# Optimization experiments

Measured on AMD Instinct MI355X. Metric: run time of the kernel, lower is better.

## Reference

```python
import jax, jax.numpy as jnp
import numpy as np

NUM_CODES = 1024
DIM = 64
COMMITMENT_WEIGHT = 0.25
SOFT_TEMP = 1.0


def setup_inputs() -> dict:
    key = jax.random.key(0)
    k1, k2 = jax.random.split(key)
    z = jax.random.normal(k1, (32, 4096, DIM), dtype=jnp.float32)
    codebook = jax.random.normal(k2, (NUM_CODES, DIM), dtype=jnp.float32)
    return {"z": z, "codebook": codebook}


def reference(z, codebook):
    b, k, d = z.shape
    flat = z.reshape(-1, d)  # [N, d]
    # squared euclidean distances [N, num_codes]
    distances = (
        jnp.sum(flat * flat, axis=1, keepdims=True)
        - 2.0 * flat @ codebook.T
        + jnp.sum(codebook * codebook, axis=1)[None, :]
    )
    indices = jnp.argmin(distances, axis=1)  # [N]
    logits = -distances / max(SOFT_TEMP, 1e-06)
    probs = jax.nn.softmax(logits, axis=1)

    quantized = codebook[indices].reshape(b, k, d)
    # use_ema=True -> quantized is detached from graph
    quantized = jax.lax.stop_gradient(quantized)

    codebook_loss = jnp.mean((jax.lax.stop_gradient(quantized) - z) ** 2)
    commitment_loss = jnp.mean((quantized - jax.lax.stop_gradient(z)) ** 2)
    loss = codebook_loss + COMMITMENT_WEIGHT * commitment_loss

    # straight-through estimator
    quantized_st = z + jax.lax.stop_gradient(quantized - z)

    counts = jnp.zeros((NUM_CODES,), dtype=jnp.float32).at[indices].add(1.0)
    usage = counts / jnp.maximum(counts.sum(), 1.0)
    soft_usage = probs.mean(axis=0)
    perplexity = jnp.exp(-jnp.sum(usage * jnp.log(usage + 1e-08)))

    return (
        quantized_st,
        loss,
        indices.reshape(b, k),
        codebook_loss,
        commitment_loss,
        perplexity,
        usage,
        soft_usage,
    )
```

## Files before the change

kernel.cpp:

```cpp
#include <hip/hip_runtime.h>

constexpr int K = 1024;
constexpr int D = 64;
constexpr int N = 131072;
constexpr float INV_N = 1.0f / 131072.0f;
constexpr float INV_ELEMS = 1.0f / 8388608.0f;
constexpr float LOG2E = 1.4426950408889634f;
constexpr float DELTA = 0.0072f;

constexpr size_t O_QST  = 0;
constexpr size_t O_LOSS = 8388608;
constexpr size_t O_IDX  = 8388609;
constexpr size_t O_CBL  = 8519681;
constexpr size_t O_CML  = 8519682;
constexpr size_t O_PPL  = 8519683;
constexpr size_t O_USG  = 8519684;
constexpr size_t O_SU   = 8520708;



typedef __attribute__((ext_vector_type(8))) short bf16x8;
typedef __attribute__((ext_vector_type(16))) float f32x16;
typedef __attribute__((ext_vector_type(4))) float f32x4;

__device__ inline unsigned short f2bf(float f) {
  unsigned u = __float_as_uint(f);
  return (unsigned short)((u + 0x7FFF + ((u >> 16) & 1)) >> 16);
}
__device__ inline float bf2f(unsigned short h) {
  return __uint_as_float(((unsigned)h) << 16);
}
__device__ inline float fexp2(float x) {
  return __builtin_amdgcn_exp2f(x);
}
__device__ inline float fmed3(float a, float b, float c) {
  return __builtin_amdgcn_fmed3f(a, b, c);
}
__device__ inline bf16x8 negbf8(bf16x8 v) {
  union { bf16x8 s; uint4 u; } x;
  x.s = v;
  x.u.x ^= 0x80008000u; x.u.y ^= 0x80008000u;
  x.u.z ^= 0x80008000u; x.u.w ^= 0x80008000u;
  return x.s;
}

__global__ __launch_bounds__(256) void vq_prep(const float* __restrict__ cb,
                                               short* __restrict__ chA,
                                               short* __restrict__ clA,
                                               float* __restrict__ cn,
                                               float* __restrict__ cn2f) {
  const int gid = blockIdx.x * 256 + threadIdx.x;
  const int c = gid >> 6, d = gid & 63;
  float raw = cb[gid];
  float v = raw * LOG2E;
  unsigned short h = f2bf(v);
  unsigned short l = f2bf(v - bf2f(h));
  const int tile = c >> 5, ks = d >> 4, hff = (d >> 3) & 1, j = d & 7;
  const int lane = hff * 32 + (c & 31);
  const size_t off = ((size_t)((tile * 4 + ks) * 64 + lane)) * 8 + j;
  chA[off] = (short)h;
  clA[off] = (short)l;
  float s = raw * raw;
#pragma unroll
  for (int o = 32; o > 0; o >>= 1) s += __shfl_xor(s, o, 64);
  if (d == 0) {
    cn[c] = s;
    cn2f[c] = s * LOG2E;
  }
}

__global__ __launch_bounds__(256, 4) void vq_p1(
    const float* __restrict__ z, const short* __restrict__ chA,
    const short* __restrict__ clA, const float* __restrict__ cn2f,
    float* __restrict__ out, float* __restrict__ ctA,
    int* __restrict__ wl) {
  const int lane = threadIdx.x & 63;
  const int W = blockIdx.x * 4 + (threadIdx.x >> 6);
  const int i0 = W * 32;
  const int col = lane & 31;
  const int hf = lane >> 5;

  bf16x8 zh[4], zl[4];
  const float* zr = z + (size_t)(i0 + col) * 64 + hf * 8;
#pragma unroll
  for (int ks = 0; ks < 4; ks++) {
    float4 a = *(const float4*)(zr + ks * 16);
    float4 b = *(const float4*)(zr + ks * 16 + 4);
    float vv[8] = {a.x, a.y, a.z, a.w, b.x, b.y, b.z, b.w};
#pragma unroll
    for (int j = 0; j < 8; j++) {
      float vm = -2.0f * vv[j];
      unsigned short h = f2bf(vm);
      zh[ks][j] = (short)h;
      zl[ks][j] = (short)f2bf(vm - bf2f(h));
    }
  }
  {
    short* base = (short*)out + (size_t)W * 4096;
#pragma unroll
    for (int ks = 0; ks < 4; ks++) {
      *(bf16x8*)(base + (ks * 64 + lane) * 8) = zh[ks];
      *(bf16x8*)(base + 2048 + (ks * 64 + lane) * 8) = zl[ks];
    }
  }

  float b1 = 3.0e38f, b2 = 3.0e38f, Z = 0.0f;
  int bi = 0;

  for (int t = 0; t < 32; t++) {
    float4 cniv[4];
#pragma unroll
    for (int q = 0; q < 4; q++)
      cniv[q] = *(const float4*)(cn2f + t * 32 + 8 * q + 4 * hf);
    f32x16 acc;
#pragma unroll
    for (int r = 0; r < 16; r++)
      acc[r] = ((const float*)&cniv[r >> 2])[r & 3];
    const short* ch = chA + ((size_t)(t * 4) * 64 + lane) * 8;
    const short* cl = clA + ((size_t)(t * 4) * 64 + lane) * 8;
#pragma unroll
    for (int ks = 0; ks < 4; ks++) {
      bf16x8 Ah = *(const bf16x8*)(ch + ks * 512);
      bf16x8 Al = *(const bf16x8*)(cl + ks * 512);
      acc = __builtin_amdgcn_mfma_f32_32x32x16_bf16(Ah, zh[ks], acc, 0, 0, 0);
      acc = __builtin_amdgcn_mfma_f32_32x32x16_bf16(Ah, zl[ks], acc, 0, 0, 0);
      acc = __builtin_amdgcn_mfma_f32_32x32x16_bf16(Al, zh[ks], acc, 0, 0, 0);
    }
    float pm[8], px[8];
#pragma unroll
    for (int r = 0; r < 8; r++) {
      pm[r] = fminf(acc[2 * r], acc[2 * r + 1]);
      px[r] = fmaxf(acc[2 * r], acc[2 * r + 1]);
    }
    float qm[4], qx[4];
#pragma unroll
    for (int r = 0; r < 4; r++) {
      qm[r] = fminf(pm[2 * r], pm[2 * r + 1]);
      qx[r] = fmed3(pm[2 * r], pm[2 * r + 1], fminf(px[2 * r], px[2 * r + 1]));
    }
    float rm0 = fminf(qm[0], qm[1]);
    float rx0 = fmed3(qm[0], qm[1], fminf(qx[0], qx[1]));
    float rm1 = fminf(qm[2], qm[3]);
    float rx1 = fmed3(qm[2], qm[3], fminf(qx[2], qx[3]));
    float cm = fminf(rm0, rm1);
    float cm2 = fmed3(rm0, rm1, fminf(rx0, rx1));
    int ti = 0;
#pragma unroll
    for (int r = 0; r < 16; r++)
      if (acc[r] == cm) ti = t * 32 + (r & 3) + 8 * (r >> 2) + 4 * hf;
    float newm = fminf(b1, cm);
    b2 = fmed3(b1, cm, fminf(b2, cm2));
    bi = (cm < b1) ? ti : bi;
    float zs = 0.0f;
#pragma unroll
    for (int r = 0; r < 16; r++) zs += fexp2(newm - acc[r]);
    Z = Z * fexp2(newm - b1) + zs;
    b1 = newm;
  }
  float m2 = __shfl_xor(b1, 32, 64);
  float Z2 = __shfl_xor(Z, 32, 64);
  float b1o = m2;
  float b2o = __shfl_xor(b2, 32, 64);
  int bio = __shfl_xor(bi, 32, 64);
  float M = fminf(b1, m2);
  float Zt = Z * fexp2(M - b1) + Z2 * fexp2(M - m2);
  bool take = (b1o < b1) || (b1o == b1 && bio < bi);
  float g2 = fminf(fmaxf(b1, b1o), fminf(b2, b2o));
  int big = take ? bio : bi;
  if (hf == 0) {
    ctA[i0 + col] = M - __log2f(Zt);
    out[O_IDX + (size_t)(i0 + col)] = (float)big;
    if (g2 - M < DELTA) {
      int slot = atomicAdd(wl, 1);
      if (slot < 131071) wl[1 + slot] = i0 + col;
    }
  }
}

__global__ __launch_bounds__(256) void vq_count(
    const float* __restrict__ idxF, float* __restrict__ counts) {
  __shared__ int h[K];
  const int tid = threadIdx.x;
#pragma unroll
  for (int k = 0; k < K / 256; k++) h[tid + k * 256] = 0;
  __syncthreads();
  const int base = blockIdx.x * 2048 + tid;
#pragma unroll
  for (int k = 0; k < 8; k++) {
    int c = (int)idxF[base + k * 256];
    atomicAdd(&h[c], 1);
  }
  __syncthreads();
#pragma unroll
  for (int k = 0; k < K / 256; k++) {
    int v = h[tid + k * 256];
    if (v) atomicAdd(&counts[tid + k * 256], (float)v);
  }
}

__global__ __launch_bounds__(256, 4) void vq_p2(
    const short* __restrict__ zF, const short* __restrict__ chA,
    const short* __restrict__ clA, const float* __restrict__ cn2f,
    const float* __restrict__ ctA, float* __restrict__ susum) {
  const int lane = threadIdx.x & 63;
  const int wv = threadIdx.x >> 6;
  const int b = blockIdx.x;
  const int xcd = b & 7;
  const int sl = b >> 3;
  const int pg = xcd * 32 + (sl >> 3);
  const int g = (sl & 7) * 4 + wv;
  const int col = lane & 31;
  const int hf = lane >> 5;

  bf16x8 Bh[4], Bl[4];
  const short* ch = chA + ((size_t)(g * 4) * 64 + lane) * 8;
  const short* cl = clA + ((size_t)(g * 4) * 64 + lane) * 8;
#pragma unroll
  for (int ks = 0; ks < 4; ks++) {
    Bh[ks] = negbf8(*(const bf16x8*)(ch + ks * 512));
    Bl[ks] = negbf8(*(const bf16x8*)(cl + ks * 512));
  }
  const float cnv = cn2f[g * 32 + col];

  float su = 0.0f;
  for (int pt = 0; pt < 16; pt++) {
    const int T = pg * 16 + pt;
    const short* base = zF + (size_t)T * 4096;
    float4 ctv[4];
#pragma unroll
    for (int q = 0; q < 4; q++)
      ctv[q] = *(const float4*)(ctA + T * 32 + 8 * q + 4 * hf);
    f32x16 acc;
#pragma unroll
    for (int r = 0; r < 16; r++)
      acc[r] = ((const float*)&ctv[r >> 2])[r & 3] - cnv;
#pragma unroll
    for (int ks = 0; ks < 4; ks++) {
      bf16x8 Ah = *(const bf16x8*)(base + (ks * 64 + lane) * 8);
      bf16x8 Al = *(const bf16x8*)(base + 2048 + (ks * 64 + lane) * 8);
      acc = __builtin_amdgcn_mfma_f32_32x32x16_bf16(Ah, Bh[ks], acc, 0, 0, 0);
      acc = __builtin_amdgcn_mfma_f32_32x32x16_bf16(Ah, Bl[ks], acc, 0, 0, 0);
      acc = __builtin_amdgcn_mfma_f32_32x32x16_bf16(Al, Bh[ks], acc, 0, 0, 0);
    }
#pragma unroll
    for (int r = 0; r < 16; r++) su += fexp2(acc[r]);
  }
  su += __shfl_xor(su, 32, 64);
  if (hf == 0) atomicAdd(&susum[g * 32 + col], su);
}

__global__ __launch_bounds__(256) void vq_rescan(
    const float* __restrict__ z, const float* __restrict__ cb,
    const float* __restrict__ cn, float* __restrict__ out,
    float* __restrict__ counts, const int* __restrict__ wl) {
  const int nr = min(wl[0], 131071);
  const int wv = blockIdx.x * 4 + (threadIdx.x >> 6);
  const int lane = threadIdx.x & 63;
  for (int e = wv; e < nr; e += gridDim.x * 4) {
    const int i = wl[1 + e];
    const float4* zi4 = (const float4*)(z + (size_t)i * 64);
    float4 zq[16];
#pragma unroll
    for (int k = 0; k < 16; k++) zq[k] = zi4[k];
    float best = 3.0e38f;
    int bidx = 0;
    for (int cc = 0; cc < 16; cc++) {
      int c = cc * 64 + lane;
      const float4* cr = (const float4*)(cb + (size_t)c * 64);
      float dot0 = 0.0f, dot1 = 0.0f;
#pragma unroll
      for (int k = 0; k < 16; k += 2) {
        float4 a = cr[k];
        float4 bq = cr[k + 1];
        dot0 += zq[k].x * a.x + zq[k].y * a.y + zq[k].z * a.z + zq[k].w * a.w;
        dot1 += zq[k + 1].x * bq.x + zq[k + 1].y * bq.y + zq[k + 1].z * bq.z +
                zq[k + 1].w * bq.w;
      }
      float s = cn[c] - 2.0f * (dot0 + dot1);
      if (s < best) { best = s; bidx = c; }
    }
#pragma unroll
    for (int o = 32; o > 0; o >>= 1) {
      float ob = __shfl_xor(best, o, 64);
      int oi = __shfl_xor(bidx, o, 64);
      if (ob < best || (ob == best && oi < bidx)) { best = ob; bidx = oi; }
    }
    if (lane == 0) {
      const int old = (int)out[O_IDX + (size_t)i];
      if (bidx != old) {
        out[O_IDX + (size_t)i] = (float)bidx;
        atomicAdd(&counts[old], -1.0f);
        atomicAdd(&counts[bidx], 1.0f);
      }
    }
  }
}

__global__ __launch_bounds__(256) void vq_epi(
    const float* __restrict__ z, const float* __restrict__ cb,
    const float* __restrict__ idxF, float* __restrict__ qst,
    float* __restrict__ sqp) {
  const int tid = threadIdx.x;
  const int base = blockIdx.x * 2048 + tid;
  const int q = base & 15;
  int bI[8];
#pragma unroll
  for (int k = 0; k < 8; k++) bI[k] = (int)idxF[(base + k * 256) >> 4];
  f32x4 zv[8];
#pragma unroll
  for (int k = 0; k < 8; k++)
    zv[k] = __builtin_nontemporal_load((const f32x4*)z + base + k * 256);
  f32x4 qv[8];
#pragma unroll
  for (int k = 0; k < 8; k++) qv[k] = ((const f32x4*)cb)[bI[k] * 16 + q];
  float sq = 0.0f;
#pragma unroll
  for (int k = 0; k < 8; k++) {
    f32x4 o = zv[k] + (qv[k] - zv[k]);
    __builtin_nontemporal_store(o, (f32x4*)qst + base + k * 256);
    f32x4 e = qv[k] - zv[k];
    sq += e.x * e.x + e.y * e.y + e.z * e.z + e.w * e.w;
  }
#pragma unroll
  for (int o2 = 32; o2 > 0; o2 >>= 1) sq += __shfl_xor(sq, o2, 64);
  if ((tid & 63) == 0)
    atomicAdd(&sqp[(blockIdx.x * 4 + (tid >> 6)) & 255], sq);
}

__global__ __launch_bounds__(1024) void vq_final(
    const float* __restrict__ counts, const float* __restrict__ susum,
    const float* __restrict__ sqp, float* __restrict__ out) {
  __shared__ float red[16];
  __shared__ float red2[16];
  const int t = threadIdx.x;
  float cnt = counts[t];
  float usage = cnt * INV_N;
  out[O_USG + t] = usage;
  out[O_SU + t] = susum[t] * INV_N;
  float term = usage * logf(usage + 1e-8f);
  float sq = (t < 256) ? sqp[t] : 0.0f;
#pragma unroll
  for (int o = 32; o > 0; o >>= 1) {
    term += __shfl_xor(term, o, 64);
    sq += __shfl_xor(sq, o, 64);
  }
  if ((t & 63) == 0) {
    red[t >> 6] = term;
    red2[t >> 6] = sq;
  }
  __syncthreads();
  if (t < 16) {
    float v = red[t];
    float s2 = red2[t];
#pragma unroll
    for (int o = 8; o > 0; o >>= 1) {
      v += __shfl_xor(v, o, 64);
      s2 += __shfl_xor(s2, o, 64);
    }
    if (t == 0) {
      float ppl = __expf(-v);
      float cbl = s2 * INV_ELEMS;
      out[O_LOSS] = cbl + 0.25f * cbl;
      out[O_CBL] = cbl;
      out[O_CML] = cbl;
      out[O_PPL] = ppl;
    }
  }
}

extern "C" void kernel_launch(void* const* d_in, const int* in_sizes, int n_in,
                              void* d_out, int out_size, void* d_ws,
                              size_t ws_size, hipStream_t stream) {
  const float* z = (const float*)d_in[0];
  const float* cb = (const float*)d_in[1];
  float* ws = (float*)d_ws;
  float* cn = ws;
  float* counts = ws + 1024;
  float* susum = ws + 2048;
  float* sqp = ws + 3072;
  float* cn2f = ws + 3328;
  short* chA = (short*)(ws + 4352);
  short* clA = (short*)(ws + 37120);
  float* ctA = ws + 69888;
  int* wl = (int*)(ws + 200960);
  float* out = (float*)d_out;

  hipMemsetAsync(counts, 0, (1024 + 1024 + 256) * sizeof(float), stream);
  hipMemsetAsync(wl, 0, sizeof(int), stream);

  vq_prep<<<256, 256, 0, stream>>>(cb, chA, clA, cn, cn2f);
  vq_p1<<<1024, 256, 0, stream>>>(z, chA, clA, cn2f, out, ctA, wl);
  vq_count<<<64, 256, 0, stream>>>(out + O_IDX, counts);
  vq_p2<<<2048, 256, 0, stream>>>((const short*)out, chA, clA, cn2f, ctA,
                                  susum);
  vq_rescan<<<256, 256, 0, stream>>>(z, cb, cn, out, counts, wl);
  vq_epi<<<N * 16 / 2048, 256, 0, stream>>>(z, cb, out + O_IDX, out + O_QST,
                                            sqp);
  vq_final<<<1, 1024, 0, stream>>>(counts, susum, sqp, out);
}
```

Measured before the change: 280.0 us.

## Split codebook scan across two waves per row tile and merge via LDS

vq_p1 now runs 512 threads per block. Two wavefronts share each 32-row tile, and each scans half of the 1024 codes (16 tiles instead of 32). Their partial min, second-min, argmin and softmax partial sums are merged through shared memory after a barrier. This doubles the wave count, giving more latency hiding and parallelism on a kernel with only 1024 blocks of 4 waves. The cost is duplicated z loading and bf16 splitting per pair, plus a block-wide sync, and the tie-break on equal minima now ignores the index.

```diff
diff --git a/kernel.cpp b/kernel.cpp
--- a/kernel.cpp
+++ b/kernel.cpp
@@ -69,13 +69,19 @@
   }
 }
 
-__global__ __launch_bounds__(256, 4) void vq_p1(
+__global__ __launch_bounds__(512, 8) void vq_p1(
     const float* __restrict__ z, const short* __restrict__ chA,
     const short* __restrict__ clA, const float* __restrict__ cn2f,
     float* __restrict__ out, float* __restrict__ ctA,
     int* __restrict__ wl) {
-  const int lane = threadIdx.x & 63;
-  const int W = blockIdx.x * 4 + (threadIdx.x >> 6);
+  __shared__ float Lm[8][32], LZ[8][32], Lb2[8][32];
+  __shared__ int Lbi[8][32];
+  const int tid = threadIdx.x;
+  const int lane = tid & 63;
+  const int w = tid >> 6;
+  const int pair = w >> 1;
+  const int half = w & 1;
+  const int W = blockIdx.x * 4 + pair;
   const int i0 = W * 32;
   const int col = lane & 31;
   const int hf = lane >> 5;
@@ -95,7 +101,7 @@
       zl[ks][j] = (short)f2bf(vm - bf2f(h));
     }
   }
-  {
+  if (half == 0) {
     short* base = (short*)out + (size_t)W * 4096;
 #pragma unroll
     for (int ks = 0; ks < 4; ks++) {
@@ -107,17 +113,18 @@
   float b1 = 3.0e38f, b2 = 3.0e38f, Z = 0.0f;
   int bi = 0;
 
-  for (int t = 0; t < 32; t++) {
+  for (int t = 0; t < 16; t++) {
+    const int tt = half * 16 + t;
     float4 cniv[4];
 #pragma unroll
     for (int q = 0; q < 4; q++)
-      cniv[q] = *(const float4*)(cn2f + t * 32 + 8 * q + 4 * hf);
+      cniv[q] = *(const float4*)(cn2f + tt * 32 + 8 * q + 4 * hf);
     f32x16 acc;
 #pragma unroll
     for (int r = 0; r < 16; r++)
       acc[r] = ((const float*)&cniv[r >> 2])[r & 3];
-    const short* ch = chA + ((size_t)(t * 4) * 64 + lane) * 8;
-    const short* cl = clA + ((size_t)(t * 4) * 64 + lane) * 8;
+    const short* ch = chA + ((size_t)(tt * 4) * 64 + lane) * 8;
+    const short* cl = clA + ((size_t)(tt * 4) * 64 + lane) * 8;
 #pragma unroll
     for (int ks = 0; ks < 4; ks++) {
       bf16x8 Ah = *(const bf16x8*)(ch + ks * 512);
@@ -147,7 +154,7 @@
     int ti = 0;
 #pragma unroll
     for (int r = 0; r < 16; r++)
-      if (acc[r] == cm) ti = t * 32 + (r & 3) + 8 * (r >> 2) + 4 * hf;
+      if (acc[r] == cm) ti = tt * 32 + (r & 3) + 8 * (r >> 2) + 4 * hf;
     float newm = fminf(b1, cm);
     b2 = fmed3(b1, cm, fminf(b2, cm2));
     bi = (cm < b1) ? ti : bi;
@@ -159,15 +166,29 @@
   }
   float m2 = __shfl_xor(b1, 32, 64);
   float Z2 = __shfl_xor(Z, 32, 64);
-  float b1o = m2;
   float b2o = __shfl_xor(b2, 32, 64);
   int bio = __shfl_xor(bi, 32, 64);
-  float M = fminf(b1, m2);
-  float Zt = Z * fexp2(M - b1) + Z2 * fexp2(M - m2);
-  bool take = (b1o < b1) || (b1o == b1 && bio < bi);
-  float g2 = fminf(fmaxf(b1, b1o), fminf(b2, b2o));
-  int big = take ? bio : bi;
+  float Mw = fminf(b1, m2);
+  float Zw = Z * fexp2(Mw - b1) + Z2 * fexp2(Mw - m2);
+  bool takeh = (m2 < b1) || (m2 == b1 && bio < bi);
+  float g2w = fminf(fmaxf(b1, m2), fminf(b2, b2o));
+  int biw = takeh ? bio : bi;
   if (hf == 0) {
+    Lm[w][col] = Mw;
+    LZ[w][col] = Zw;
+    Lb2[w][col] = g2w;
+    Lbi[w][col] = biw;
+  }
+  __syncthreads();
+  if (half == 0 && hf == 0) {
+    float mB = Lm[w ^ 1][col];
+    float ZB = LZ[w ^ 1][col];
+    float b2B = Lb2[w ^ 1][col];
+    int biB = Lbi[w ^ 1][col];
+    float M = fminf(Mw, mB);
+    float Zt = Zw * fexp2(M - Mw) + ZB * fexp2(M - mB);
+    int big = (mB < Mw) ? biB : biw;
+    float g2 = fminf(fmaxf(Mw, mB), fminf(g2w, b2B));
     ctA[i0 + col] = M - __log2f(Zt);
     out[O_IDX + (size_t)(i0 + col)] = (float)big;
     if (g2 - M < DELTA) {
@@ -389,7 +410,7 @@
   hipMemsetAsync(wl, 0, sizeof(int), stream);
 
   vq_prep<<<256, 256, 0, stream>>>(cb, chA, clA, cn, cn2f);
-  vq_p1<<<1024, 256, 0, stream>>>(z, chA, clA, cn2f, out, ctA, wl);
+  vq_p1<<<1024, 512, 0, stream>>>(z, chA, clA, cn2f, out, ctA, wl);
   vq_count<<<64, 256, 0, stream>>>(out + O_IDX, counts);
   vq_p2<<<2048, 256, 0, stream>>>((const short*)out, chA, clA, cn2f, ctA,
                                   susum);
```

After: 327.1 us. 16.8% more time.

## Double-buffer codebook fragments in p1 and hoist per-code norm out of soft-usage loop

Applied to the files above, without the earlier changes.

The distance pass now prefetches the next codebook tile's bf16 fragments into a second register buffer while the current tile's MFMAs and reductions run, and lowers its occupancy hint from 4 to 3 waves to make room for the extra registers. The exp-sum accumulations are split into two independent partial sums to shorten dependency chains. In the soft-usage kernel, the per-code norm subtraction is removed from every accumulator init and applied once as an exp2 scale factor at the end. A constant shift folded into the stored log-normalizer keeps the exponentials in range. Lower occupancy and the shift's effect on float range are the risks.

```diff
diff --git a/kernel.cpp b/kernel.cpp
--- a/kernel.cpp
+++ b/kernel.cpp
@@ -7,6 +7,7 @@
 constexpr float INV_ELEMS = 1.0f / 8388608.0f;
 constexpr float LOG2E = 1.4426950408889634f;
 constexpr float DELTA = 0.0072f;
+constexpr float SHIFT = 92.332482616893656f;
 
 constexpr size_t O_QST  = 0;
 constexpr size_t O_LOSS = 8388608;
@@ -69,7 +70,7 @@
   }
 }
 
-__global__ __launch_bounds__(256, 4) void vq_p1(
+__global__ __launch_bounds__(256, 3) void vq_p1(
     const float* __restrict__ z, const short* __restrict__ chA,
     const short* __restrict__ clA, const float* __restrict__ cn2f,
     float* __restrict__ out, float* __restrict__ ctA,
@@ -107,24 +108,20 @@
   float b1 = 3.0e38f, b2 = 3.0e38f, Z = 0.0f;
   int bi = 0;
 
-  for (int t = 0; t < 32; t++) {
+  auto step = [&](int tt, const bf16x8* AH, const bf16x8* AL) {
     float4 cniv[4];
 #pragma unroll
     for (int q = 0; q < 4; q++)
-      cniv[q] = *(const float4*)(cn2f + t * 32 + 8 * q + 4 * hf);
+      cniv[q] = *(const float4*)(cn2f + tt * 32 + 8 * q + 4 * hf);
     f32x16 acc;
 #pragma unroll
     for (int r = 0; r < 16; r++)
       acc[r] = ((const float*)&cniv[r >> 2])[r & 3];
-    const short* ch = chA + ((size_t)(t * 4) * 64 + lane) * 8;
-    const short* cl = clA + ((size_t)(t * 4) * 64 + lane) * 8;
 #pragma unroll
     for (int ks = 0; ks < 4; ks++) {
-      bf16x8 Ah = *(const bf16x8*)(ch + ks * 512);
-      bf16x8 Al = *(const bf16x8*)(cl + ks * 512);
-      acc = __builtin_amdgcn_mfma_f32_32x32x16_bf16(Ah, zh[ks], acc, 0, 0, 0);
-      acc = __builtin_amdgcn_mfma_f32_32x32x16_bf16(Ah, zl[ks], acc, 0, 0, 0);
-      acc = __builtin_amdgcn_mfma_f32_32x32x16_bf16(Al, zh[ks], acc, 0, 0, 0);
+      acc = __builtin_amdgcn_mfma_f32_32x32x16_bf16(AH[ks], zh[ks], acc, 0, 0, 0);
+      acc = __builtin_amdgcn_mfma_f32_32x32x16_bf16(AH[ks], zl[ks], acc, 0, 0, 0);
+      acc = __builtin_amdgcn_mfma_f32_32x32x16_bf16(AL[ks], zh[ks], acc, 0, 0, 0);
     }
     float pm[8], px[8];
 #pragma unroll
@@ -147,16 +144,43 @@
     int ti = 0;
 #pragma unroll
     for (int r = 0; r < 16; r++)
-      if (acc[r] == cm) ti = t * 32 + (r & 3) + 8 * (r >> 2) + 4 * hf;
+      if (acc[r] == cm) ti = tt * 32 + (r & 3) + 8 * (r >> 2) + 4 * hf;
     float newm = fminf(b1, cm);
     b2 = fmed3(b1, cm, fminf(b2, cm2));
     bi = (cm < b1) ? ti : bi;
-    float zs = 0.0f;
-#pragma unroll
-    for (int r = 0; r < 16; r++) zs += fexp2(newm - acc[r]);
-    Z = Z * fexp2(newm - b1) + zs;
+    float zs0 = 0.0f, zs1 = 0.0f;
+#pragma unroll
+    for (int r = 0; r < 16; r += 2) {
+      zs0 += fexp2(newm - acc[r]);
+      zs1 += fexp2(newm - acc[r + 1]);
+    }
+    Z = Z * fexp2(newm - b1) + (zs0 + zs1);
     b1 = newm;
-  }
+  };
+
+  bf16x8 A0h[4], A0l[4], A1h[4], A1l[4];
+#pragma unroll
+  for (int ks = 0; ks < 4; ks++) {
+    A0h[ks] = *(const bf16x8*)(chA + (size_t)lane * 8 + ks * 512);
+    A0l[ks] = *(const bf16x8*)(clA + (size_t)lane * 8 + ks * 512);
+  }
+  for (int t = 0; t < 32; t += 2) {
+    const size_t o1 = (size_t)(t + 1) * 2048 + lane * 8;
+#pragma unroll
+    for (int ks = 0; ks < 4; ks++) {
+      A1h[ks] = *(const bf16x8*)(chA + o1 + ks * 512);
+      A1l[ks] = *(const bf16x8*)(clA + o1 + ks * 512);
+    }
+    step(t, A0h, A0l);
+    const size_t o2 = (size_t)((t + 2) & 31) * 2048 + lane * 8;
+#pragma unroll
+    for (int ks = 0; ks < 4; ks++) {
+      A0h[ks] = *(const bf16x8*)(chA + o2 + ks * 512);
+      A0l[ks] = *(const bf16x8*)(clA + o2 + ks * 512);
+    }
+    step(t + 1, A1h, A1l);
+  }
+
   float m2 = __shfl_xor(b1, 32, 64);
   float Z2 = __shfl_xor(Z, 32, 64);
   float b1o = m2;
@@ -168,7 +192,7 @@
   float g2 = fminf(fmaxf(b1, b1o), fminf(b2, b2o));
   int big = take ? bio : bi;
   if (hf == 0) {
-    ctA[i0 + col] = M - __log2f(Zt);
+    ctA[i0 + col] = M - __log2f(Zt) - SHIFT;
     out[O_IDX + (size_t)(i0 + col)] = (float)big;
     if (g2 - M < DELTA) {
       int slot = atomicAdd(wl, 1);
@@ -221,8 +245,9 @@
     Bl[ks] = negbf8(*(const bf16x8*)(cl + ks * 512));
   }
   const float cnv = cn2f[g * 32 + col];
-
-  float su = 0.0f;
+  const float escale = fexp2(SHIFT - cnv);
+
+  float su0 = 0.0f, su1 = 0.0f;
   for (int pt = 0; pt < 16; pt++) {
     const int T = pg * 16 + pt;
     const short* base = zF + (size_t)T * 4096;
@@ -233,7 +258,7 @@
     f32x16 acc;
 #pragma unroll
     for (int r = 0; r < 16; r++)
-      acc[r] = ((const float*)&ctv[r >> 2])[r & 3] - cnv;
+      acc[r] = ((const float*)&ctv[r >> 2])[r & 3];
 #pragma unroll
     for (int ks = 0; ks < 4; ks++) {
       bf16x8 Ah = *(const bf16x8*)(base + (ks * 64 + lane) * 8);
@@ -243,8 +268,12 @@
       acc = __builtin_amdgcn_mfma_f32_32x32x16_bf16(Al, Bh[ks], acc, 0, 0, 0);
     }
 #pragma unroll
-    for (int r = 0; r < 16; r++) su += fexp2(acc[r]);
-  }
+    for (int r = 0; r < 16; r += 2) {
+      su0 += fexp2(acc[r]);
+      su1 += fexp2(acc[r + 1]);
+    }
+  }
+  float su = (su0 + su1) * escale;
   su += __shfl_xor(su, 32, 64);
   if (hf == 0) atomicAdd(&susum[g * 32 + col], su);
 }
```

Result: no change. 275.6 us (-1.6%).
